# Kernel tuning notes

Hardware: AMD Instinct MI355X
Metric: run time of the kernel (lower is better)

The kernel has to match this reference:

```python
import jax, jax.numpy as jnp
import numpy as np

B, C, H, W = 16, 256, 64, 64
K = 1024

def setup_inputs() -> dict:
    key = jax.random.key(0)
    k1, k2 = jax.random.split(key)
    x = jax.random.normal(k1, (B, C, H, W), dtype=jnp.float32)
    codebook = jax.random.normal(k2, (K, C), dtype=jnp.float32)
    return {"x": x, "codebook": codebook}


def reference(x, codebook):
    b, c, h, w = x.shape
    # (B, C, H, W) -> (B*H*W, C)
    xf = jnp.transpose(x, (0, 2, 3, 1)).reshape(-1, c)
    # Squared euclidean distances to codebook (argmin is the same as for cdist).
    x2 = jnp.sum(xf * xf, axis=-1, keepdims=True)          # (N, 1)
    c2 = jnp.sum(codebook * codebook, axis=-1)               # (K,)
    dist = x2 - 2.0 * jnp.einsum('nc,kc->nk', xf, codebook) + c2  # (N, K)
    idx = jnp.argmin(dist, axis=-1)                          # (N,)
    quant = codebook[idx]                                     # (N, C)
    commitment_loss = jnp.mean((jax.lax.stop_gradient(quant) - xf) ** 2)
    codebook_loss = jnp.mean((quant - jax.lax.stop_gradient(xf)) ** 2)
    # Straight-through estimator
    quant_out = xf + jax.lax.stop_gradient(quant - xf)
    quant_out = jnp.transpose(quant_out.reshape(b, h, w, c), (0, 3, 1, 2))
    indices = idx.reshape(b, h, w)
    return quant_out, codebook_loss, commitment_loss, indices
```

## Files before the change

### kernel.cpp

```cpp
#include <hip/hip_runtime.h>

constexpr int Bn = 16, Cd = 256, Hn = 64, Wn = 64, Kc = 1024;
constexpr int QUANT_ELEMS = Bn * Hn * Wn * Cd;
constexpr int LOSS_OFF = QUANT_ELEMS;
constexpr int IDX_OFF = QUANT_ELEMS + 2;

typedef _Float16 half8 __attribute__((ext_vector_type(8)));
typedef float f32x4 __attribute__((ext_vector_type(4)));

constexpr size_t WS_CBFH = 0;
constexpr size_t WS_CBFL = 512 * 1024;
constexpr size_t WS_C2   = 1024 * 1024;
constexpr size_t WS_CNT  = 1024 * 1024 + 4096;
constexpr size_t WS_ROWS = 1024 * 1024 + 8192;
constexpr size_t WS_IDX  = 1024 * 1024 + 8192 + 262144;
constexpr size_t WS_CBT  = 1024 * 1024 + 8192 + 524288;

__global__ __launch_bounds__(256) void prep(const float* __restrict__ cb,
                                            float* __restrict__ cbT,
                                            _Float16* __restrict__ cbFh,
                                            _Float16* __restrict__ cbFl,
                                            float* __restrict__ c2,
                                            int* __restrict__ cnt,
                                            float* __restrict__ out) {
    __shared__ float cbs[64][257];
    const int tid = threadIdx.x;
    const int k0 = blockIdx.x * 64;
    {
        const int c4 = (tid & 63) * 4;
        const int r0 = tid >> 6;
        #pragma unroll
        for (int it = 0; it < 16; ++it) {
            const int r = r0 + it * 4;
            const float4 v = *(const float4*)&cb[(size_t)(k0 + r) * Cd + c4];
            cbs[r][c4] = v.x; cbs[r][c4 + 1] = v.y; cbs[r][c4 + 2] = v.z; cbs[r][c4 + 3] = v.w;
        }
    }
    __syncthreads();
    {
        const int kk = tid & 63, j0 = tid >> 6;
        for (int j = j0; j < 256; j += 4)
            cbT[(size_t)j * Kc + k0 + kk] = cbs[kk][j];
    }
    {
        const int i = tid >> 2, part = tid & 3;
        float s = 0.f;
        for (int c = part * 64; c < part * 64 + 64; ++c) { const float v = cbs[i][c]; s += v * v; }
        s += __shfl_xor(s, 1);
        s += __shfl_xor(s, 2);
        if (part == 0) c2[k0 + i] = s;
    }
    for (int t = tid; t < 2048; t += 256) {
        const int ntl = t >> 9;
        const int kblk = (t >> 6) & 7;
        const int l = t & 63;
        const int code_l = ntl * 16 + (l & 15);
        const int cbase = kblk * 32 + (l >> 4) * 8;
        half8 hv, lv;
        #pragma unroll
        for (int j = 0; j < 8; ++j) {
            const float v = cbs[code_l][cbase + j];
            const _Float16 hh = (_Float16)v;
            hv[j] = hh;
            lv[j] = (_Float16)(v - (float)hh);
        }
        const size_t e = (size_t)(((k0 >> 4) + ntl) * 8 + kblk) * 64 + l;
        *(half8*)(cbFh + e * 8) = hv;
        *(half8*)(cbFl + e * 8) = lv;
    }
    if (blockIdx.x == 0 && tid == 0) {
        cnt[0] = 0; out[LOSS_OFF] = 0.f; out[LOSS_OFF + 1] = 0.f;
    }
}

__global__ __launch_bounds__(256, 2) void vq_main(const float* __restrict__ x,
                                                  const _Float16* __restrict__ cbFh,
                                                  const _Float16* __restrict__ cbFl,
                                                  const float* __restrict__ c2,
                                                  const float* __restrict__ cb,
                                                  float* __restrict__ out,
                                                  int* __restrict__ idx_int,
                                                  int* __restrict__ cnt,
                                                  int* __restrict__ rows) {
    __shared__ half8 Axh[2048];
    __shared__ half8 Axl[2048];
    __shared__ float q1ds[4][64];
    __shared__ int   q1is[4][64];
    __shared__ float q2ds[4][64];
    __shared__ int   idx_s[64];
    __shared__ float red[4];

    const int tid = threadIdx.x;
    const int lane = tid & 63;
    const int wv = tid >> 6;
    const int bh = blockIdx.x;
    const int b = bh >> 6, h = bh & 63;

    {
        const int m = tid & 15;
        const int q = (tid >> 4) & 3;
        const int mt = tid >> 6;
        const int w = mt * 16 + m;
        const float* xb = x + ((size_t)b * Cd * Hn + h) * Wn + w;
        #pragma unroll
        for (int kblk = 0; kblk < 8; ++kblk) {
            half8 hv, lv;
            #pragma unroll
            for (int j = 0; j < 8; ++j) {
                const int c = kblk * 32 + q * 8 + j;
                const float v = xb[(size_t)c * (Hn * Wn)];
                const _Float16 hh = (_Float16)v;
                hv[j] = hh;
                lv[j] = (_Float16)(v - (float)hh);
            }
            const int e = (kblk * 4 + mt) * 64 + (q * 16 + m);
            Axh[e] = hv;
            Axl[e] = lv;
        }
    }
    __syncthreads();

    float q1d[16], q2d[16];
    int   q1i[16];
    #pragma unroll
    for (int i = 0; i < 16; ++i) { q1d[i] = 3.4e38f; q2d[i] = 3.4e38f; q1i[i] = 0; }

    #pragma unroll 1
    for (int grp = 0; grp < 4; ++grp) {
        f32x4 acc[4][4];
        #pragma unroll
        for (int mt = 0; mt < 4; ++mt)
            #pragma unroll
            for (int nt = 0; nt < 4; ++nt) acc[mt][nt] = (f32x4){0.f, 0.f, 0.f, 0.f};

        #pragma unroll 2
        for (int kblk = 0; kblk < 8; ++kblk) {
            half8 bhf[4], blf[4];
            #pragma unroll
            for (int nt = 0; nt < 4; ++nt) {
                const int ntile = wv * 16 + grp * 4 + nt;
                const size_t be = ((size_t)(ntile * 8 + kblk) * 64 + lane) * 8;
                bhf[nt] = *(const half8*)(cbFh + be);
                blf[nt] = *(const half8*)(cbFl + be);
            }
            half8 ahf[4];
            #pragma unroll
            for (int mt = 0; mt < 4; ++mt) {
                const int e = (kblk * 4 + mt) * 64 + lane;
                ahf[mt] = Axh[e];
            }
            #pragma unroll
            for (int nt = 0; nt < 4; ++nt)
                #pragma unroll
                for (int mt = 0; mt < 4; ++mt)
                    acc[mt][nt] = __builtin_amdgcn_mfma_f32_16x16x32_f16(ahf[mt], bhf[nt], acc[mt][nt], 0, 0, 0);
            #pragma unroll
            for (int nt = 0; nt < 4; ++nt)
                #pragma unroll
                for (int mt = 0; mt < 4; ++mt)
                    acc[mt][nt] = __builtin_amdgcn_mfma_f32_16x16x32_f16(ahf[mt], blf[nt], acc[mt][nt], 0, 0, 0);
        }

        #pragma unroll
        for (int nt = 0; nt < 4; ++nt) {
            const int code = (wv * 16 + grp * 4 + nt) * 16 + (lane & 15);
            const float c2v = c2[code];
            #pragma unroll
            for (int mt = 0; mt < 4; ++mt) {
                #pragma unroll
                for (int reg = 0; reg < 4; ++reg) {
                    const float d = fmaf(-2.f, acc[mt][nt][reg], c2v);
                    const int qi = mt * 4 + reg;
                    const bool better = d < q1d[qi];
                    const float second = better ? q1d[qi] : d;
                    q2d[qi] = fminf(q2d[qi], second);
                    q1i[qi] = better ? code : q1i[qi];
                    q1d[qi] = fminf(q1d[qi], d);
                }
            }
        }
    }

    #pragma unroll
    for (int off = 1; off < 16; off <<= 1) {
        #pragma unroll
        for (int qi = 0; qi < 16; ++qi) {
            const float od1 = __shfl_xor(q1d[qi], off);
            const int   oi1 = __shfl_xor(q1i[qi], off);
            const float od2 = __shfl_xor(q2d[qi], off);
            const bool obetter = od1 < q1d[qi];
            const float loser = obetter ? q1d[qi] : od1;
            q2d[qi] = fminf(fminf(q2d[qi], od2), loser);
            q1d[qi] = obetter ? od1 : q1d[qi];
            q1i[qi] = obetter ? oi1 : q1i[qi];
        }
    }
    if ((lane & 15) == 0) {
        #pragma unroll
        for (int qi = 0; qi < 16; ++qi) {
            const int mt = qi >> 2, reg = qi & 3;
            const int row = mt * 16 + (lane >> 4) * 4 + reg;
            q1ds[wv][row] = q1d[qi];
            q1is[wv][row] = q1i[qi];
            q2ds[wv][row] = q2d[qi];
        }
    }
    __syncthreads();
    if (tid < 64) {
        float d1 = q1ds[0][tid]; int i1 = q1is[0][tid]; float d2 = q2ds[0][tid];
        #pragma unroll
        for (int v = 1; v < 4; ++v) {
            const float od1 = q1ds[v][tid]; const int oi1 = q1is[v][tid]; const float od2 = q2ds[v][tid];
            const bool obetter = od1 < d1;
            const float loser = obetter ? d1 : od1;
            d2 = fminf(fminf(d2, od2), loser);
            d1 = obetter ? od1 : d1;
            i1 = obetter ? oi1 : i1;
        }
        const int grow = bh * 64 + tid;
        idx_s[tid] = i1;
        idx_int[grow] = i1;
        out[IDX_OFF + grow] = (float)i1;
        if (d2 - d1 < 0.12f) {
            const int pos = atomicAdd(cnt, 1);
            rows[pos] = grow;
        }
    }
    __syncthreads();

    {
        const int w = tid & 63;
        const int cq = wv;
        const int m = w & 15, mt = w >> 4;
        const int myidx = idx_s[w];
        const float4* cbrow = (const float4*)(cb + (size_t)myidx * Cd + cq * 64);
        float lsum = 0.f;
        #pragma unroll
        for (int half = 0; half < 2; ++half) {
            const int kblk = cq * 2 + half;
            #pragma unroll
            for (int q = 0; q < 4; ++q) {
                const int e = (kblk * 4 + mt) * 64 + q * 16 + m;
                const half8 hv = Axh[e];
                const half8 lv = Axl[e];
                const float4 qa = cbrow[half * 8 + q * 2];
                const float4 qb = cbrow[half * 8 + q * 2 + 1];
                const float qv[8] = {qa.x, qa.y, qa.z, qa.w, qb.x, qb.y, qb.z, qb.w};
                const int cbase = cq * 64 + half * 32 + q * 8;
                #pragma unroll
                for (int j = 0; j < 8; ++j) {
                    const float xv = (float)hv[j] + (float)lv[j];
                    const float dd = qv[j] - xv;
                    lsum += dd * dd;
                    out[(((size_t)b * Cd + cbase + j) * Hn + h) * Wn + w] = qv[j];
                }
            }
        }
        #pragma unroll
        for (int off = 32; off >= 1; off >>= 1) lsum += __shfl_xor(lsum, off);
        if (lane == 0) red[wv] = lsum;
    }
    __syncthreads();
    if (tid == 0) {
        const float s = (red[0] + red[1] + red[2] + red[3]) * (1.0f / 16777216.0f);
        atomicAdd(out + LOSS_OFF, s);
        atomicAdd(out + LOSS_OFF + 1, s);
    }
}

__global__ __launch_bounds__(256) void fixup(const float* __restrict__ x,
                                             const float* __restrict__ cbT,
                                             const float* __restrict__ cb,
                                             const float* __restrict__ c2,
                                             const int* __restrict__ cnt,
                                             const int* __restrict__ rows,
                                             float* __restrict__ out,
                                             int* __restrict__ idx_int) {
    __shared__ float xs[256];
    __shared__ float ds[256];
    __shared__ int kk[256];
    __shared__ int s_old;
    const int t = threadIdx.x;
    const int n = cnt[0];
    for (int i = blockIdx.x; i < n; i += gridDim.x) {
        const int row = rows[i];
        const int b = row >> 12, h = (row >> 6) & 63, w = row & 63;
        __syncthreads();
        xs[t] = x[(((size_t)b * Cd + t) * Hn + h) * Wn + w];
        if (t == 0) s_old = idx_int[row];
        __syncthreads();
        float dot[4] = {0.f, 0.f, 0.f, 0.f};
        #pragma unroll 8
        for (int c = 0; c < Cd; ++c) {
            const float4 v = ((const float4*)(cbT + (size_t)c * Kc))[t];
            const float xc = xs[c];
            dot[0] = fmaf(v.x, xc, dot[0]);
            dot[1] = fmaf(v.y, xc, dot[1]);
            dot[2] = fmaf(v.z, xc, dot[2]);
            dot[3] = fmaf(v.w, xc, dot[3]);
        }
        float bd = 3.4e38f; int bk = 0;
        #pragma unroll
        for (int j = 0; j < 4; ++j) {
            const int k = t * 4 + j;
            const float d = c2[k] - 2.f * dot[j];
            if (d < bd) { bd = d; bk = k; }
        }
        ds[t] = bd; kk[t] = bk;
        __syncthreads();
        for (int s = 128; s > 0; s >>= 1) {
            if (t < s) {
                const float od = ds[t + s]; const int ok = kk[t + s];
                if (od < ds[t] || (od == ds[t] && ok < kk[t])) { ds[t] = od; kk[t] = ok; }
            }
            __syncthreads();
        }
        const int kn = kk[0], ko = s_old;
        if (t == 0 && kn != ko) { idx_int[row] = kn; out[IDX_OFF + row] = (float)kn; }
        if (kn != ko) {
            const float qn = cb[(size_t)kn * Cd + t];
            const float qo = cb[(size_t)ko * Cd + t];
            const float xv = xs[t];
            const float dn = qn - xv, dold = qo - xv;
            float delta = dn * dn - dold * dold;
            out[(((size_t)b * Cd + t) * Hn + h) * Wn + w] = qn;
            #pragma unroll
            for (int off = 32; off >= 1; off >>= 1) delta += __shfl_xor(delta, off);
            ds[t] = 0.f;
            __syncthreads();
            if ((t & 63) == 0) ds[t >> 6] = delta;
            __syncthreads();
            if (t == 0) {
                const float s = (ds[0] + ds[1] + ds[2] + ds[3]) * (1.0f / 16777216.0f);
                atomicAdd(out + LOSS_OFF, s);
                atomicAdd(out + LOSS_OFF + 1, s);
            }
        }
    }
}

extern "C" void kernel_launch(void* const* d_in, const int* in_sizes, int n_in,
                              void* d_out, int out_size, void* d_ws, size_t ws_size,
                              hipStream_t stream) {
    const float* x  = (const float*)d_in[0];
    const float* cb = (const float*)d_in[1];
    float* out = (float*)d_out;
    char* ws = (char*)d_ws;
    _Float16* cbFh = (_Float16*)(ws + WS_CBFH);
    _Float16* cbFl = (_Float16*)(ws + WS_CBFL);
    float* c2      = (float*)(ws + WS_C2);
    int* cnt       = (int*)(ws + WS_CNT);
    int* rows      = (int*)(ws + WS_ROWS);
    int* idx_int   = (int*)(ws + WS_IDX);
    float* cbT     = (float*)(ws + WS_CBT);

    prep<<<16, 256, 0, stream>>>(cb, cbT, cbFh, cbFl, c2, cnt, out);
    vq_main<<<Bn * Hn, 256, 0, stream>>>(x, cbFh, cbFl, c2, cb, out, idx_int, cnt, rows);
    fixup<<<256, 256, 0, stream>>>(x, cbT, cb, c2, cnt, rows, out, idx_int);
}
```

Baseline: 263.6 us.

## Fuse exact-refinement fixup into main VQ kernel and drop x low-half split

Moves the fp32 re-check of ambiguous rows from a separate fixup kernel into vq_main, so each block refines its own flagged rows from shared memory before writing quantized output once. The fp16 low-part of x is removed (only the codebook keeps its hi/lo split), which halves the activation LDS footprint and allows raising the occupancy hint to 4 blocks per CU. The output and loss pass now reads x directly from global memory instead of reconstructing it from LDS. The prep kernel is split across 64 smaller blocks. The risk is that blocks with many flagged rows serialize the per-row refinement and cause load imbalance.

```diff
diff --git a/kernel.cpp b/kernel.cpp
--- a/kernel.cpp
+++ b/kernel.cpp
@@ -11,26 +11,22 @@
 constexpr size_t WS_CBFH = 0;
 constexpr size_t WS_CBFL = 512 * 1024;
 constexpr size_t WS_C2   = 1024 * 1024;
-constexpr size_t WS_CNT  = 1024 * 1024 + 4096;
-constexpr size_t WS_ROWS = 1024 * 1024 + 8192;
-constexpr size_t WS_IDX  = 1024 * 1024 + 8192 + 262144;
-constexpr size_t WS_CBT  = 1024 * 1024 + 8192 + 524288;
+constexpr size_t WS_CBT  = 1024 * 1024 + 8192;
 
 __global__ __launch_bounds__(256) void prep(const float* __restrict__ cb,
                                             float* __restrict__ cbT,
                                             _Float16* __restrict__ cbFh,
                                             _Float16* __restrict__ cbFl,
                                             float* __restrict__ c2,
-                                            int* __restrict__ cnt,
                                             float* __restrict__ out) {
-    __shared__ float cbs[64][257];
+    __shared__ float cbs[16][257];
     const int tid = threadIdx.x;
-    const int k0 = blockIdx.x * 64;
+    const int k0 = blockIdx.x * 16;
     {
         const int c4 = (tid & 63) * 4;
         const int r0 = tid >> 6;
         #pragma unroll
-        for (int it = 0; it < 16; ++it) {
+        for (int it = 0; it < 4; ++it) {
             const int r = r0 + it * 4;
             const float4 v = *(const float4*)&cb[(size_t)(k0 + r) * Cd + c4];
             cbs[r][c4] = v.x; cbs[r][c4 + 1] = v.y; cbs[r][c4 + 2] = v.z; cbs[r][c4 + 3] = v.w;
@@ -38,23 +34,25 @@
     }
     __syncthreads();
     {
-        const int kk = tid & 63, j0 = tid >> 6;
-        for (int j = j0; j < 256; j += 4)
+        const int kk = tid & 15, j0 = tid >> 4;
+        for (int j = j0; j < 256; j += 16)
             cbT[(size_t)j * Kc + k0 + kk] = cbs[kk][j];
     }
     {
-        const int i = tid >> 2, part = tid & 3;
+        const int i = tid >> 4, part = tid & 15;
         float s = 0.f;
-        for (int c = part * 64; c < part * 64 + 64; ++c) { const float v = cbs[i][c]; s += v * v; }
+        #pragma unroll
+        for (int c = part * 16; c < part * 16 + 16; ++c) { const float v = cbs[i][c]; s += v * v; }
         s += __shfl_xor(s, 1);
         s += __shfl_xor(s, 2);
+        s += __shfl_xor(s, 4);
+        s += __shfl_xor(s, 8);
         if (part == 0) c2[k0 + i] = s;
     }
-    for (int t = tid; t < 2048; t += 256) {
-        const int ntl = t >> 9;
-        const int kblk = (t >> 6) & 7;
+    for (int t = tid; t < 512; t += 256) {
+        const int kblk = t >> 6;
         const int l = t & 63;
-        const int code_l = ntl * 16 + (l & 15);
+        const int code_l = l & 15;
         const int cbase = kblk * 32 + (l >> 4) * 8;
         half8 hv, lv;
         #pragma unroll
@@ -64,31 +62,34 @@
             hv[j] = hh;
             lv[j] = (_Float16)(v - (float)hh);
         }
-        const size_t e = (size_t)(((k0 >> 4) + ntl) * 8 + kblk) * 64 + l;
+        const size_t e = (size_t)(blockIdx.x * 8 + kblk) * 64 + l;
         *(half8*)(cbFh + e * 8) = hv;
         *(half8*)(cbFl + e * 8) = lv;
     }
     if (blockIdx.x == 0 && tid == 0) {
-        cnt[0] = 0; out[LOSS_OFF] = 0.f; out[LOSS_OFF + 1] = 0.f;
+        out[LOSS_OFF] = 0.f; out[LOSS_OFF + 1] = 0.f;
     }
 }
 
-__global__ __launch_bounds__(256, 2) void vq_main(const float* __restrict__ x,
+__global__ __launch_bounds__(256, 4) void vq_main(const float* __restrict__ x,
                                                   const _Float16* __restrict__ cbFh,
                                                   const _Float16* __restrict__ cbFl,
                                                   const float* __restrict__ c2,
                                                   const float* __restrict__ cb,
-                                                  float* __restrict__ out,
-                                                  int* __restrict__ idx_int,
-                                                  int* __restrict__ cnt,
-                                                  int* __restrict__ rows) {
+                                                  const float* __restrict__ cbT,
+                                                  float* __restrict__ out) {
     __shared__ half8 Axh[2048];
-    __shared__ half8 Axl[2048];
     __shared__ float q1ds[4][64];
     __shared__ int   q1is[4][64];
     __shared__ float q2ds[4][64];
     __shared__ int   idx_s[64];
     __shared__ float red[4];
+    __shared__ int   flg[64];
+    __shared__ int   nflag;
+
+    float* xs  = (float*)Axh;
+    float* dsm = xs + 256;
+    int*   kkm = (int*)(dsm + 256);
 
     const int tid = threadIdx.x;
     const int lane = tid & 63;
@@ -96,6 +97,8 @@
     const int bh = blockIdx.x;
     const int b = bh >> 6, h = bh & 63;
 
+    if (tid == 0) nflag = 0;
+
     {
         const int m = tid & 15;
         const int q = (tid >> 4) & 3;
@@ -104,18 +107,14 @@
         const float* xb = x + ((size_t)b * Cd * Hn + h) * Wn + w;
         #pragma unroll
         for (int kblk = 0; kblk < 8; ++kblk) {
-            half8 hv, lv;
+            half8 hv;
             #pragma unroll
             for (int j = 0; j < 8; ++j) {
                 const int c = kblk * 32 + q * 8 + j;
                 const float v = xb[(size_t)c * (Hn * Wn)];
-                const _Float16 hh = (_Float16)v;
-                hv[j] = hh;
-                lv[j] = (_Float16)(v - (float)hh);
+                hv[j] = (_Float16)v;
             }
-            const int e = (kblk * 4 + mt) * 64 + (q * 16 + m);
-            Axh[e] = hv;
-            Axl[e] = lv;
+            Axh[(kblk * 4 + mt) * 64 + (q * 16 + m)] = hv;
         }
     }
     __syncthreads();
@@ -145,10 +144,8 @@
             }
             half8 ahf[4];
             #pragma unroll
-            for (int mt = 0; mt < 4; ++mt) {
-                const int e = (kblk * 4 + mt) * 64 + lane;
-                ahf[mt] = Axh[e];
-            }
+            for (int mt = 0; mt < 4; ++mt)
+                ahf[mt] = Axh[(kblk * 4 + mt) * 64 + lane];
             #pragma unroll
             for (int nt = 0; nt < 4; ++nt)
                 #pragma unroll
@@ -217,82 +214,23 @@
             d1 = obetter ? od1 : d1;
             i1 = obetter ? oi1 : i1;
         }
-        const int grow = bh * 64 + tid;
         idx_s[tid] = i1;
-        idx_int[grow] = i1;
-        out[IDX_OFF + grow] = (float)i1;
         if (d2 - d1 < 0.12f) {
-            const int pos = atomicAdd(cnt, 1);
-            rows[pos] = grow;
-        }
-    }
-    __syncthreads();
-
-    {
-        const int w = tid & 63;
-        const int cq = wv;
-        const int m = w & 15, mt = w >> 4;
-        const int myidx = idx_s[w];
-        const float4* cbrow = (const float4*)(cb + (size_t)myidx * Cd + cq * 64);
-        float lsum = 0.f;
-        #pragma unroll
-        for (int half = 0; half < 2; ++half) {
-            const int kblk = cq * 2 + half;
-            #pragma unroll
-            for (int q = 0; q < 4; ++q) {
-                const int e = (kblk * 4 + mt) * 64 + q * 16 + m;
-                const half8 hv = Axh[e];
-                const half8 lv = Axl[e];
-                const float4 qa = cbrow[half * 8 + q * 2];
-                const float4 qb = cbrow[half * 8 + q * 2 + 1];
-                const float qv[8] = {qa.x, qa.y, qa.z, qa.w, qb.x, qb.y, qb.z, qb.w};
-                const int cbase = cq * 64 + half * 32 + q * 8;
-                #pragma unroll
-                for (int j = 0; j < 8; ++j) {
-                    const float xv = (float)hv[j] + (float)lv[j];
-                    const float dd = qv[j] - xv;
-                    lsum += dd * dd;
-                    out[(((size_t)b * Cd + cbase + j) * Hn + h) * Wn + w] = qv[j];
-                }
-            }
-        }
-        #pragma unroll
-        for (int off = 32; off >= 1; off >>= 1) lsum += __shfl_xor(lsum, off);
-        if (lane == 0) red[wv] = lsum;
-    }
-    __syncthreads();
-    if (tid == 0) {
-        const float s = (red[0] + red[1] + red[2] + red[3]) * (1.0f / 16777216.0f);
-        atomicAdd(out + LOSS_OFF, s);
-        atomicAdd(out + LOSS_OFF + 1, s);
-    }
-}
-
-__global__ __launch_bounds__(256) void fixup(const float* __restrict__ x,
-                                             const float* __restrict__ cbT,
-                                             const float* __restrict__ cb,
-                                             const float* __restrict__ c2,
-                                             const int* __restrict__ cnt,
-                                             const int* __restrict__ rows,
-                                             float* __restrict__ out,
-                                             int* __restrict__ idx_int) {
-    __shared__ float xs[256];
-    __shared__ float ds[256];
-    __shared__ int kk[256];
-    __shared__ int s_old;
-    const int t = threadIdx.x;
-    const int n = cnt[0];
-    for (int i = blockIdx.x; i < n; i += gridDim.x) {
-        const int row = rows[i];
-        const int b = row >> 12, h = (row >> 6) & 63, w = row & 63;
-        __syncthreads();
-        xs[t] = x[(((size_t)b * Cd + t) * Hn + h) * Wn + w];
-        if (t == 0) s_old = idx_int[row];
+            const int pos = atomicAdd(&nflag, 1);
+            flg[pos] = tid;
+        }
+    }
+    __syncthreads();
+
+    const int nf = nflag;
+    for (int fi = 0; fi < nf; ++fi) {
+        const int wrow = flg[fi];
+        xs[tid] = x[(((size_t)b * Cd + tid) * Hn + h) * Wn + wrow];
         __syncthreads();
         float dot[4] = {0.f, 0.f, 0.f, 0.f};
         #pragma unroll 8
         for (int c = 0; c < Cd; ++c) {
-            const float4 v = ((const float4*)(cbT + (size_t)c * Kc))[t];
+            const float4 v = ((const float4*)(cbT + (size_t)c * Kc))[tid];
             const float xc = xs[c];
             dot[0] = fmaf(v.x, xc, dot[0]);
             dot[1] = fmaf(v.y, xc, dot[1]);
@@ -302,40 +240,57 @@
         float bd = 3.4e38f; int bk = 0;
         #pragma unroll
         for (int j = 0; j < 4; ++j) {
-            const int k = t * 4 + j;
+            const int k = tid * 4 + j;
             const float d = c2[k] - 2.f * dot[j];
             if (d < bd) { bd = d; bk = k; }
         }
-        ds[t] = bd; kk[t] = bk;
+        dsm[tid] = bd; kkm[tid] = bk;
         __syncthreads();
         for (int s = 128; s > 0; s >>= 1) {
-            if (t < s) {
-                const float od = ds[t + s]; const int ok = kk[t + s];
-                if (od < ds[t] || (od == ds[t] && ok < kk[t])) { ds[t] = od; kk[t] = ok; }
+            if (tid < s) {
+                const float od = dsm[tid + s]; const int ok = kkm[tid + s];
+                if (od < dsm[tid] || (od == dsm[tid] && ok < kkm[tid])) { dsm[tid] = od; kkm[tid] = ok; }
             }
             __syncthreads();
         }
-        const int kn = kk[0], ko = s_old;
-        if (t == 0 && kn != ko) { idx_int[row] = kn; out[IDX_OFF + row] = (float)kn; }
-        if (kn != ko) {
-            const float qn = cb[(size_t)kn * Cd + t];
-            const float qo = cb[(size_t)ko * Cd + t];
-            const float xv = xs[t];
-            const float dn = qn - xv, dold = qo - xv;
-            float delta = dn * dn - dold * dold;
-            out[(((size_t)b * Cd + t) * Hn + h) * Wn + w] = qn;
-            #pragma unroll
-            for (int off = 32; off >= 1; off >>= 1) delta += __shfl_xor(delta, off);
-            ds[t] = 0.f;
-            __syncthreads();
-            if ((t & 63) == 0) ds[t >> 6] = delta;
-            __syncthreads();
-            if (t == 0) {
-                const float s = (ds[0] + ds[1] + ds[2] + ds[3]) * (1.0f / 16777216.0f);
-                atomicAdd(out + LOSS_OFF, s);
-                atomicAdd(out + LOSS_OFF + 1, s);
-            }
-        }
+        if (tid == 0) idx_s[wrow] = kkm[0];
+        __syncthreads();
+    }
+
+    if (tid < 64) out[IDX_OFF + bh * 64 + tid] = (float)idx_s[tid];
+
+    {
+        const int w = tid & 63;
+        const int cq = wv;
+        const int myidx = idx_s[w];
+        const float4* cbrow = (const float4*)(cb + (size_t)myidx * Cd + cq * 64);
+        const float* xrow = x + (((size_t)b * Cd + cq * 64) * Hn + h) * Wn + w;
+        float* orow = out + (((size_t)b * Cd + cq * 64) * Hn + h) * Wn + w;
+        float lsum = 0.f;
+        #pragma unroll
+        for (int i = 0; i < 16; ++i) {
+            const float4 qv4 = cbrow[i];
+            const size_t c0 = (size_t)(i * 4) * (Hn * Wn);
+            const float xv0 = xrow[c0];
+            const float xv1 = xrow[c0 + 1 * (Hn * Wn)];
+            const float xv2 = xrow[c0 + 2 * (Hn * Wn)];
+            const float xv3 = xrow[c0 + 3 * (Hn * Wn)];
+            const float d0 = qv4.x - xv0, d1 = qv4.y - xv1, d2 = qv4.z - xv2, d3 = qv4.w - xv3;
+            lsum += d0 * d0 + d1 * d1 + d2 * d2 + d3 * d3;
+            orow[c0] = qv4.x;
+            orow[c0 + 1 * (Hn * Wn)] = qv4.y;
+            orow[c0 + 2 * (Hn * Wn)] = qv4.z;
+            orow[c0 + 3 * (Hn * Wn)] = qv4.w;
+        }
+        #pragma unroll
+        for (int off = 32; off >= 1; off >>= 1) lsum += __shfl_xor(lsum, off);
+        if (lane == 0) red[wv] = lsum;
+    }
+    __syncthreads();
+    if (tid == 0) {
+        const float s = (red[0] + red[1] + red[2] + red[3]) * (1.0f / 16777216.0f);
+        atomicAdd(out + LOSS_OFF, s);
+        atomicAdd(out + LOSS_OFF + 1, s);
     }
 }
 
@@ -349,12 +304,8 @@
     _Float16* cbFh = (_Float16*)(ws + WS_CBFH);
     _Float16* cbFl = (_Float16*)(ws + WS_CBFL);
     float* c2      = (float*)(ws + WS_C2);
-    int* cnt       = (int*)(ws + WS_CNT);
-    int* rows      = (int*)(ws + WS_ROWS);
-    int* idx_int   = (int*)(ws + WS_IDX);
     float* cbT     = (float*)(ws + WS_CBT);
 
-    prep<<<16, 256, 0, stream>>>(cb, cbT, cbFh, cbFl, c2, cnt, out);
-    vq_main<<<Bn * Hn, 256, 0, stream>>>(x, cbFh, cbFl, c2, cb, out, idx_int, cnt, rows);
-    fixup<<<256, 256, 0, stream>>>(x, cbT, cb, c2, cnt, rows, out, idx_int);
+    prep<<<64, 256, 0, stream>>>(cb, cbT, cbFh, cbFl, c2, out);
+    vq_main<<<Bn * Hn, 256, 0, stream>>>(x, cbFh, cbFl, c2, cb, cbT, out);
 }
```

After: 310.8 us. 17.9% more time.
